# Performance work log

Hardware: AMD Instinct MI355X
Metric: run time of the kernel (lower is better)

Reference implementation:

```python
import jax, jax.numpy as jnp
import numpy as np

EPS = 1e-05
POOL = 10  # pooling_kernel

def setup_inputs() -> dict:
    key = jax.random.key(0)
    x = jax.random.normal(key, (8, 16, 2000, 128), dtype=jnp.float32)
    return {"x": x}

def reference(x) -> jnp.ndarray:
    B, C, T, F = x.shape
    # (B, C, T, F) -> (B, C*F, T), matching permute(0,1,3,2).reshape
    xr = jnp.transpose(x, (0, 1, 3, 2)).reshape(B, C * F, T)
    T1 = T // POOL
    # pooled block means of x and x^2 (AvgPool1d kernel=stride=POOL)
    blocks = xr[:, :, : T1 * POOL].reshape(B, C * F, T1, POOL)
    pm = blocks.mean(-1)            # (B, CF, T1)
    pm2 = (blocks ** 2).mean(-1)    # (B, CF, T1)
    # causal cumulative mean over pooled blocks (replaces O(T1^2) mask-multiply)
    nfrms = jnp.arange(1, T1 + 1, dtype=xr.dtype)  # (T1,)
    cmean = jnp.cumsum(pm, axis=-1) / nfrms
    cmean2 = jnp.cumsum(pm2, axis=-1) / nfrms
    var = cmean2 - cmean ** 2
    # repeat each block stat POOL times along time
    mean_t = jnp.repeat(cmean, POOL, axis=-1)  # (B, CF, T1*POOL)
    var_t = jnp.repeat(var, POOL, axis=-1)
    if T1 * POOL < T:  # pad tail with last stat (static branch)
        pad = T - T1 * POOL
        mean_t = jnp.concatenate([mean_t, jnp.repeat(mean_t[:, :, -1:], pad, axis=-1)], axis=-1)
        var_t = jnp.concatenate([var_t, jnp.repeat(var_t[:, :, -1:], pad, axis=-1)], axis=-1)
    x_norm = (xr - mean_t) / jnp.sqrt(var_t + EPS)
    # (B, CF, T) -> (B, C, F, T) -> (B, C, T, F)
    return jnp.transpose(x_norm.reshape(B, C, F, T), (0, 1, 3, 2))
```

## Files before the change

### kernel.cpp

```cpp
#include <hip/hip_runtime.h>

#define B_    8
#define C_    16
#define T_    2000
#define F_    128
#define POOL_ 10
#define T1_   200
#define BC_   (B_*C_)
#define EPS_  1e-5f

__global__ __launch_bounds__(256) void k1_blocksums(
    const float4* __restrict__ x4, float4* __restrict__ S4, float4* __restrict__ S24)
{
    int bid = blockIdx.x;
    int bc  = bid / (T1_ / 8);
    int t1  = (bid % (T1_ / 8)) * 8 + (threadIdx.x >> 5);
    int f4  = threadIdx.x & 31;

    const float4* p = x4 + (size_t)(bc * T_ + t1 * POOL_) * (F_ / 4) + f4;
    float4 s  = {0.f, 0.f, 0.f, 0.f};
    float4 s2 = {0.f, 0.f, 0.f, 0.f};
#pragma unroll
    for (int k = 0; k < POOL_; ++k) {
        float4 v = p[(size_t)k * (F_ / 4)];
        s.x += v.x; s.y += v.y; s.z += v.z; s.w += v.w;
        s2.x = fmaf(v.x, v.x, s2.x);
        s2.y = fmaf(v.y, v.y, s2.y);
        s2.z = fmaf(v.z, v.z, s2.z);
        s2.w = fmaf(v.w, v.w, s2.w);
    }
    size_t o = (size_t)(bc * T1_ + t1) * (F_ / 4) + f4;
    S4[o]  = s;
    S24[o] = s2;
}

__global__ __launch_bounds__(64) void k2_scan(
    float* __restrict__ S, float* __restrict__ S2)
{
    int g  = blockIdx.x * 64 + threadIdx.x;
    int bc = g / F_;
    int f  = g - bc * F_;

    float rs = 0.f, rs2 = 0.f;
    size_t idx = (size_t)bc * T1_ * F_ + f;
#pragma unroll 4
    for (int t1 = 0; t1 < T1_; ++t1, idx += F_) {
        rs  += S[idx];
        rs2 += S2[idx];
        float inv = 1.0f / (float)((t1 + 1) * POOL_);
        float m   = rs  * inv;
        float m2  = rs2 * inv;
        float var = m2 - m * m;
        S[idx]  = m;
        S2[idx] = rsqrtf(var + EPS_);
    }
}

__global__ __launch_bounds__(256) void k3_norm(
    const float4* __restrict__ x4, const float4* __restrict__ M4,
    const float4* __restrict__ R4, float4* __restrict__ out4)
{
    int gid = blockIdx.x * 256 + threadIdx.x;
    int f4  = gid & (F_ / 4 - 1);
    int tmp = gid >> 5;
    int t   = tmp % T_;
    int bc  = tmp / T_;

    size_t sidx = (size_t)(bc * T1_ + t / POOL_) * (F_ / 4) + f4;
    float4 xv = x4[gid];
    float4 m  = M4[sidx];
    float4 r  = R4[sidx];
    float4 o;
    o.x = (xv.x - m.x) * r.x;
    o.y = (xv.y - m.y) * r.y;
    o.z = (xv.z - m.z) * r.z;
    o.w = (xv.w - m.w) * r.w;
    out4[gid] = o;
}

extern "C" void kernel_launch(void* const* d_in, const int* in_sizes, int n_in,
                              void* d_out, int out_size, void* d_ws, size_t ws_size,
                              hipStream_t stream)
{
    const float* x   = (const float*)d_in[0];
    float*       out = (float*)d_out;

    float* S  = (float*)d_ws;
    float* S2 = S + (size_t)BC_ * T1_ * F_;

    k1_blocksums<<<BC_ * (T1_ / 8), 256, 0, stream>>>(
        (const float4*)x, (float4*)S, (float4*)S2);

    k2_scan<<<BC_ * F_ / 64, 64, 0, stream>>>(S, S2);

    k3_norm<<<(BC_ * T_ * (F_ / 4)) / 256, 256, 0, stream>>>(
        (const float4*)x, (const float4*)S, (const float4*)S2, (float4*)out);
}
```

Before: 273.9 us.

## Fuse blocksum, scan and normalize into one kernel with decoupled look-back

Replaces three kernels with a single kernel. Each workgroup computes pooled sums for a chunk of 40 pooled frames, does an in-block prefix scan, and obtains the carry from earlier chunks via a decoupled look-back with atomic flags. It then normalizes its own chunk, re-reading x while it is likely still cache-resident. This removes the launch overhead, the global S/S2 round trips and the slow serial scan kernel. The cost is inter-block spin-waiting and a dependency on all blocks being co-resident.

```diff
diff --git a/kernel.cpp b/kernel.cpp
--- a/kernel.cpp
+++ b/kernel.cpp
@@ -1,81 +1,177 @@
 #include <hip/hip_runtime.h>
+#include <stdint.h>
 
-#define B_    8
-#define C_    16
 #define T_    2000
-#define F_    128
+#define F4_   32
 #define POOL_ 10
-#define T1_   200
-#define BC_   (B_*C_)
+#define BC_   128
 #define EPS_  1e-5f
+#define CPB_  5
+#define CH_   40
+#define L_    5
+#define NCHUNK_ 640
 
-__global__ __launch_bounds__(256) void k1_blocksums(
-    const float4* __restrict__ x4, float4* __restrict__ S4, float4* __restrict__ S24)
-{
-    int bid = blockIdx.x;
-    int bc  = bid / (T1_ / 8);
-    int t1  = (bid % (T1_ / 8)) * 8 + (threadIdx.x >> 5);
-    int f4  = threadIdx.x & 31;
 
-    const float4* p = x4 + (size_t)(bc * T_ + t1 * POOL_) * (F_ / 4) + f4;
-    float4 s  = {0.f, 0.f, 0.f, 0.f};
-    float4 s2 = {0.f, 0.f, 0.f, 0.f};
-#pragma unroll
-    for (int k = 0; k < POOL_; ++k) {
-        float4 v = p[(size_t)k * (F_ / 4)];
-        s.x += v.x; s.y += v.y; s.z += v.z; s.w += v.w;
-        s2.x = fmaf(v.x, v.x, s2.x);
-        s2.y = fmaf(v.y, v.y, s2.y);
-        s2.z = fmaf(v.z, v.z, s2.z);
-        s2.w = fmaf(v.w, v.w, s2.w);
-    }
-    size_t o = (size_t)(bc * T1_ + t1) * (F_ / 4) + f4;
-    S4[o]  = s;
-    S24[o] = s2;
+__device__ __forceinline__ void atom_st_f(float* p, float v) {
+    __hip_atomic_store((unsigned int*)p, __float_as_uint(v),
+                       __ATOMIC_RELAXED, __HIP_MEMORY_SCOPE_AGENT);
+}
+__device__ __forceinline__ float atom_ld_f(const float* p) {
+    return __uint_as_float(__hip_atomic_load((const unsigned int*)p,
+                       __ATOMIC_RELAXED, __HIP_MEMORY_SCOPE_AGENT));
 }
 
-__global__ __launch_bounds__(64) void k2_scan(
-    float* __restrict__ S, float* __restrict__ S2)
+__global__ __launch_bounds__(256, 2) void fused_cin(
+    const float4* __restrict__ x4, float4* __restrict__ out4,
+    unsigned int* __restrict__ hdr, float* __restrict__ pay)
 {
-    int g  = blockIdx.x * 64 + threadIdx.x;
-    int bc = g / F_;
-    int f  = g - bc * F_;
+    __shared__ unsigned int s_vid;
+    __shared__ float4 lsS[8][32], lsS2[8][32];
+    __shared__ float4 lbS[32], lbS2[32];
 
-    float rs = 0.f, rs2 = 0.f;
-    size_t idx = (size_t)bc * T1_ * F_ + f;
-#pragma unroll 4
-    for (int t1 = 0; t1 < T1_; ++t1, idx += F_) {
-        rs  += S[idx];
-        rs2 += S2[idx];
-        float inv = 1.0f / (float)((t1 + 1) * POOL_);
-        float m   = rs  * inv;
-        float m2  = rs2 * inv;
-        float var = m2 - m * m;
-        S[idx]  = m;
-        S2[idx] = rsqrtf(var + EPS_);
+    const int tid = threadIdx.x;
+    if (tid == 0) s_vid = atomicAdd(hdr, 1u);
+    __syncthreads();
+    const unsigned int vid = s_vid;
+    const int bc = vid & (BC_ - 1);
+    const int c  = vid >> 7;
+    const int g  = tid >> 5;
+    const int l  = tid & 31;
+
+    unsigned int* flags = hdr + 64;
+    float* aggS  = pay;
+    float* aggS2 = pay + (size_t)NCHUNK_ * 128;
+    float* incS  = pay + (size_t)2 * NCHUNK_ * 128;
+    float* incS2 = pay + (size_t)3 * NCHUNK_ * 128;
+
+    float4 iS[L_], iS2[L_];
+    float4 aggAcc = {0,0,0,0}, aggAcc2 = {0,0,0,0};
+    const int t1_0 = c * CH_;
+#pragma unroll
+    for (int it = 0; it < L_; ++it) {
+        const int t1 = t1_0 + it * 8 + g;
+        const float4* p = x4 + (size_t)(bc * T_ + t1 * POOL_) * F4_ + l;
+        float4 s = {0,0,0,0}, s2 = {0,0,0,0};
+#pragma unroll
+        for (int k = 0; k < POOL_; ++k) {
+            float4 v = p[k * F4_];
+            s.x += v.x; s.y += v.y; s.z += v.z; s.w += v.w;
+            s2.x = fmaf(v.x, v.x, s2.x);
+            s2.y = fmaf(v.y, v.y, s2.y);
+            s2.z = fmaf(v.z, v.z, s2.z);
+            s2.w = fmaf(v.w, v.w, s2.w);
+        }
+        __syncthreads();
+        lsS[g][l] = s; lsS2[g][l] = s2;
+        __syncthreads();
+        float4 run = aggAcc, run2 = aggAcc2;
+        float4 mine = run, mine2 = run2;
+#pragma unroll
+        for (int gg = 0; gg < 8; ++gg) {
+            float4 a = lsS[gg][l], a2 = lsS2[gg][l];
+            run.x += a.x; run.y += a.y; run.z += a.z; run.w += a.w;
+            run2.x += a2.x; run2.y += a2.y; run2.z += a2.z; run2.w += a2.w;
+            if (gg == g) { mine = run; mine2 = run2; }
+        }
+        iS[it] = mine; iS2[it] = mine2;
+        aggAcc = run; aggAcc2 = run2;
     }
-}
 
-__global__ __launch_bounds__(256) void k3_norm(
-    const float4* __restrict__ x4, const float4* __restrict__ M4,
-    const float4* __restrict__ R4, float4* __restrict__ out4)
-{
-    int gid = blockIdx.x * 256 + threadIdx.x;
-    int f4  = gid & (F_ / 4 - 1);
-    int tmp = gid >> 5;
-    int t   = tmp % T_;
-    int bc  = tmp / T_;
+    const size_t rec = (size_t)vid * 128 + 4 * l;
+    const bool last = (c == CPB_ - 1);
+    if (!last && tid < 64) {
+        if (tid < 32) {
+            atom_st_f(&aggS[rec + 0], aggAcc.x);
+            atom_st_f(&aggS[rec + 1], aggAcc.y);
+            atom_st_f(&aggS[rec + 2], aggAcc.z);
+            atom_st_f(&aggS[rec + 3], aggAcc.w);
+        } else {
+            atom_st_f(&aggS2[rec + 0], aggAcc2.x);
+            atom_st_f(&aggS2[rec + 1], aggAcc2.y);
+            atom_st_f(&aggS2[rec + 2], aggAcc2.z);
+            atom_st_f(&aggS2[rec + 3], aggAcc2.w);
+        }
+        if (tid == 0) {
+            __threadfence();
+            __hip_atomic_store(&flags[vid], 1u, __ATOMIC_RELEASE,
+                               __HIP_MEMORY_SCOPE_AGENT);
+        }
+    }
 
-    size_t sidx = (size_t)(bc * T1_ + t / POOL_) * (F_ / 4) + f4;
-    float4 xv = x4[gid];
-    float4 m  = M4[sidx];
-    float4 r  = R4[sidx];
-    float4 o;
-    o.x = (xv.x - m.x) * r.x;
-    o.y = (xv.y - m.y) * r.y;
-    o.z = (xv.z - m.z) * r.z;
-    o.w = (xv.w - m.w) * r.w;
-    out4[gid] = o;
+    if (tid < 64) {
+        float4 carry = {0,0,0,0};
+        const int half = tid >> 5;
+        const float* aggA = half ? aggS2 : aggS;
+        const float* incA = half ? incS2 : incS;
+        for (int cc = c - 1; cc >= 0; --cc) {
+            const unsigned int pv = (unsigned int)(cc * BC_ + bc);
+            unsigned int f;
+            while ((f = __hip_atomic_load(&flags[pv], __ATOMIC_ACQUIRE,
+                                          __HIP_MEMORY_SCOPE_AGENT)) == 0u)
+                __builtin_amdgcn_s_sleep(1);
+            const size_t r = (size_t)pv * 128 + 4 * l;
+            const float* src = (f == 2u) ? incA : aggA;
+            carry.x += atom_ld_f(&src[r + 0]);
+            carry.y += atom_ld_f(&src[r + 1]);
+            carry.z += atom_ld_f(&src[r + 2]);
+            carry.w += atom_ld_f(&src[r + 3]);
+            if (f == 2u) break;
+        }
+        if (half == 0) lbS[l] = carry; else lbS2[l] = carry;
+        if (!last) {
+            float4 inc;
+            if (half == 0) {
+                inc.x = carry.x + aggAcc.x; inc.y = carry.y + aggAcc.y;
+                inc.z = carry.z + aggAcc.z; inc.w = carry.w + aggAcc.w;
+                atom_st_f(&incS[rec + 0], inc.x);
+                atom_st_f(&incS[rec + 1], inc.y);
+                atom_st_f(&incS[rec + 2], inc.z);
+                atom_st_f(&incS[rec + 3], inc.w);
+            } else {
+                inc.x = carry.x + aggAcc2.x; inc.y = carry.y + aggAcc2.y;
+                inc.z = carry.z + aggAcc2.z; inc.w = carry.w + aggAcc2.w;
+                atom_st_f(&incS2[rec + 0], inc.x);
+                atom_st_f(&incS2[rec + 1], inc.y);
+                atom_st_f(&incS2[rec + 2], inc.z);
+                atom_st_f(&incS2[rec + 3], inc.w);
+            }
+            if (tid == 0) {
+                __threadfence();
+                __hip_atomic_store(&flags[vid], 2u, __ATOMIC_RELEASE,
+                                   __HIP_MEMORY_SCOPE_AGENT);
+            }
+        }
+    }
+    __syncthreads();
+
+    const float4 bS = lbS[l], bS2 = lbS2[l];
+#pragma unroll
+    for (int it = 0; it < L_; ++it) {
+        const int t1 = t1_0 + it * 8 + g;
+        const float invn = 1.0f / (float)((t1 + 1) * POOL_);
+        float4 m, r;
+        m.x = (iS[it].x + bS.x) * invn;
+        m.y = (iS[it].y + bS.y) * invn;
+        m.z = (iS[it].z + bS.z) * invn;
+        m.w = (iS[it].w + bS.w) * invn;
+        r.x = rsqrtf(fmaf(-m.x, m.x, (iS2[it].x + bS2.x) * invn) + EPS_);
+        r.y = rsqrtf(fmaf(-m.y, m.y, (iS2[it].y + bS2.y) * invn) + EPS_);
+        r.z = rsqrtf(fmaf(-m.z, m.z, (iS2[it].z + bS2.z) * invn) + EPS_);
+        r.w = rsqrtf(fmaf(-m.w, m.w, (iS2[it].w + bS2.w) * invn) + EPS_);
+        const size_t off = (size_t)(bc * T_ + t1 * POOL_) * F4_ + l;
+        const float4* p = x4 + off;
+        float4* q = out4 + off;
+#pragma unroll
+        for (int k = 0; k < POOL_; ++k) {
+            float4 v = p[k * F4_];
+            float4 o;
+            o.x = (v.x - m.x) * r.x;
+            o.y = (v.y - m.y) * r.y;
+            o.z = (v.z - m.z) * r.z;
+            o.w = (v.w - m.w) * r.w;
+            q[k * F4_] = o;
+        }
+    }
 }
 
 extern "C" void kernel_launch(void* const* d_in, const int* in_sizes, int n_in,
@@ -85,14 +181,11 @@
     const float* x   = (const float*)d_in[0];
     float*       out = (float*)d_out;
 
-    float* S  = (float*)d_ws;
-    float* S2 = S + (size_t)BC_ * T1_ * F_;
+    hipMemsetAsync(d_ws, 0, 4096, stream);
 
-    k1_blocksums<<<BC_ * (T1_ / 8), 256, 0, stream>>>(
-        (const float4*)x, (float4*)S, (float4*)S2);
+    unsigned int* hdr = (unsigned int*)d_ws;
+    float*        pay = (float*)((char*)d_ws + 4096);
 
-    k2_scan<<<BC_ * F_ / 64, 64, 0, stream>>>(S, S2);
-
-    k3_norm<<<(BC_ * T_ * (F_ / 4)) / 256, 256, 0, stream>>>(
-        (const float4*)x, (const float4*)S, (const float4*)S2, (float4*)out);
+    fused_cin<<<NCHUNK_, 256, 0, stream>>>(
+        (const float4*)x, (float4*)out, hdr, pay);
 }
```

Result: slower. 368.8 us (+34.6%).
